# Performance work log

Hardware: AMD Instinct MI355X
Metric: run time of the kernel (lower is better)

The kernel has to match this reference:

```python
import jax, jax.numpy as jnp
import numpy as np

MIN_NORM = 1e-15
N = 10000        # num_nodes
E = 320000       # num edges (avg degree 32)
F_IN = 512       # in_features
HID = 256        # hardcoded encoder hidden dim
D_HYP = 2        # Poincare embedding dim
HEIGHT = 2
MAX_SIZE = 0.999
MIN_SCALE = HEIGHT * (MAX_SIZE / (HEIGHT + 1))  # = 0.666, scale clamp lower bound
MAX_SCALE = MAX_SIZE


def setup_inputs() -> dict:
    key = jax.random.key(0)
    ks = jax.random.split(key, 5)
    feature = jax.random.normal(ks[0], (N, F_IN), jnp.float32)
    edge_index = jax.random.randint(ks[1], (2, E), 0, N, dtype=jnp.int64)
    W1 = jax.random.normal(ks[2], (F_IN, HID), jnp.float32) / np.sqrt(F_IN).astype(np.float32)
    b1 = jnp.zeros((HID,), jnp.float32)
    W2 = jax.random.normal(ks[3], (HID, D_HYP), jnp.float32) / np.sqrt(HID).astype(np.float32)
    b2 = jnp.zeros((D_HYP,), jnp.float32)
    scale = jnp.ones((1,), jnp.float32)  # init_size overridden to 1.0 in __init__
    return {"feature": feature, "edge_index": edge_index, "W1": W1, "b1": b1,
            "W2": W2, "b2": b2, "scale": scale}


def _gcn_agg(h, src, dst):
    # symmetric-normalized edge_index gather/aggregate (message passing)
    deg = jax.ops.segment_sum(jnp.ones((src.shape[0],), h.dtype), dst, num_segments=N)
    deg = jnp.maximum(deg, 1.0)
    norm = jax.lax.rsqrt(deg[src] * deg[dst])            # [E]
    msg = h[src] * norm[:, None]                          # [E, C] gather (irregular)
    return jax.ops.segment_sum(msg, dst, num_segments=N)  # [N, C] scatter-add


def reference(feature, edge_index, W1, b1, W2, b2, scale):
    src, dst = edge_index[0], edge_index[1]
    # 2-layer graph encoder (linear -> aggregate -> relu, linear -> aggregate)
    h = jax.nn.relu(_gcn_agg(feature @ W1 + b1, src, dst))   # [N, HID]
    u = _gcn_agg(h @ W2 + b2, src, dst)                      # [N, D_HYP] tangent at origin
    # lift to Lorentz model (k=-1) via expmap0: x = [cosh|u|, sinh|u| * u/|u|]
    un = jnp.maximum(jnp.linalg.norm(u, axis=-1, keepdims=True), MIN_NORM)
    x_l = jnp.concatenate([jnp.cosh(un), jnp.sinh(un) * u / un], axis=-1)  # [N, D_HYP+1]
    # Lorentz -> Poincare: p = x_space / (1 + x_time)
    p = x_l[:, 1:] / (1.0 + x_l[:, :1])
    # normalize: F.normalize(p, dim=-1) * scale.clamp(min_size, max_size)
    pn = jnp.maximum(jnp.linalg.norm(p, axis=-1, keepdims=True), 1e-12)
    s = jnp.clip(scale, MIN_SCALE, MAX_SCALE)
    p = p / pn * s
    # project onto Poincare ball of curvature k=-1 with eps=MIN_NORM
    norm = jnp.maximum(jnp.linalg.norm(p, axis=-1, keepdims=True), MIN_NORM)
    maxnorm = 1.0 - MIN_NORM
    return jnp.where(norm > maxnorm, p / norm * maxnorm, p)
```

## Files before the change

kernel.cpp:

```cpp
#include <hip/hip_runtime.h>
#include <math.h>

#define N_NODES 10000
#define N_EDGES 320000
#define F_IN 512
#define HID 256
#define PAD_DEG 80
#define N_GEMM_BLKS 632
#define BUILD_BLKS ((N_EDGES + 255) / 256)

typedef _Float16 half8 __attribute__((ext_vector_type(8)));
typedef _Float16 half4v __attribute__((ext_vector_type(4)));
typedef float floatx4 __attribute__((ext_vector_type(4)));

typedef const __attribute__((address_space(1))) void* gas_ptr;
typedef __attribute__((address_space(3))) void* las_ptr;

__device__ __forceinline__ void dma16(const void* g, void* l) {
    __builtin_amdgcn_global_load_lds((gas_ptr)g, (las_ptr)l, 16, 0, 0);
}

__device__ __forceinline__ void fma4(float4& acc, float s, const float4& v) {
    acc.x += s * v.x; acc.y += s * v.y; acc.z += s * v.z; acc.w += s * v.w;
}

__device__ __forceinline__ float4 h4_to_f4(half4v h) {
    float4 f; f.x = (float)h[0]; f.y = (float)h[1]; f.z = (float)h[2]; f.w = (float)h[3];
    return f;
}


__global__ __launch_bounds__(256) void k_pre(const float* __restrict__ W1,
                                             int* __restrict__ count,
                                             _Float16* __restrict__ Bt_hi,
                                             _Float16* __restrict__ Bt_lo) {
    int i = blockIdx.x * blockDim.x + threadIdx.x;
    if (i < 10240) count[i] = 0;
    int k = i >> 8, n = i & 255;
    float v = W1[i];
    _Float16 hi = (_Float16)v;
    Bt_hi[n * F_IN + k] = hi;
    Bt_lo[n * F_IN + k] = (_Float16)(v - (float)hi);
}


__global__ __launch_bounds__(256) void k_main(const float* __restrict__ A,
                                              const _Float16* __restrict__ Bt_hi,
                                              const _Float16* __restrict__ Bt_lo,
                                              const float* __restrict__ b1,
                                              _Float16* __restrict__ h0h,
                                              const int* __restrict__ ei,
                                              int* __restrict__ count,
                                              int* __restrict__ csr) {
    __shared__ float    As[4][2048];
    __shared__ _Float16 Bhs[4][2048];
    __shared__ _Float16 Bls[4][2048];
    const int tid = threadIdx.x;

    if (blockIdx.x >= N_GEMM_BLKS) {
        int e = (blockIdx.x - N_GEMM_BLKS) * 256 + tid;
        if (e < N_EDGES) {
            int src = ei[e];
            int dst = ei[N_EDGES + e];
            int pos = atomicAdd(&count[dst], 1);
            csr[dst * PAD_DEG + pos] = src;
        }
        return;
    }

    const int b = blockIdx.x;
    const int t = (b & 7) * 79 + (b >> 3);
    const int row0 = (t >> 2) * 64, col0 = (t & 3) * 64;

    const int sA0 = tid, sA1 = tid + 256;
    const int rA0 = sA0 >> 3, hA0 = (sA0 & 7) ^ (rA0 & 7);
    const int rA1 = sA1 >> 3, hA1 = (sA1 & 7) ^ (rA1 & 7);
    int gr0 = row0 + rA0; if (gr0 > N_NODES - 1) gr0 = N_NODES - 1;
    int gr1 = row0 + rA1; if (gr1 > N_NODES - 1) gr1 = N_NODES - 1;
    const float* gA0 = A + (size_t)gr0 * F_IN + hA0 * 4;
    const float* gA1 = A + (size_t)gr1 * F_IN + hA1 * 4;
    const int cB = tid >> 2, hB = (tid & 3) ^ (cB & 3);
    const _Float16* gBh = Bt_hi + (size_t)(col0 + cB) * F_IN + hB * 8;
    const _Float16* gBl = Bt_lo + (size_t)(col0 + cB) * F_IN + hB * 8;

    const int wdma = __builtin_amdgcn_readfirstlane(tid >> 6);
    char* lA  = (char*)&As[0][0];
    char* lBh = (char*)&Bhs[0][0];
    char* lBl = (char*)&Bls[0][0];
    const int dA0u = wdma * 1024;
    const int dA1u = 4096 + wdma * 1024;
    const int dBu  = wdma * 1024;

    dma16(gA0, lA + dA0u);
    dma16(gA1, lA + dA1u);
    dma16(gBh, lBh + dBu);
    dma16(gBl, lBl + dBu);
    dma16(gA0 + 32, lA  + 8192 + dA0u);
    dma16(gA1 + 32, lA  + 8192 + dA1u);
    dma16(gBh + 32, lBh + 4096 + dBu);
    dma16(gBl + 32, lBl + 4096 + dBu);

    const int lane = tid & 63, w = tid >> 6;
    const int quad = lane >> 4, l15 = lane & 15;
    const int wm = (w >> 1) * 32, wn = (w & 1) * 32;
    floatx4 acc[2][2] = {};

    int aoff[2][2], boff[2];
    #pragma unroll
    for (int mi = 0; mi < 2; ++mi) {
        int r = wm + mi * 16 + l15;
        aoff[mi][0] = r * 128 + ((2 * quad)     ^ (r & 7)) * 16;
        aoff[mi][1] = r * 128 + ((2 * quad + 1) ^ (r & 7)) * 16;
    }
    #pragma unroll
    for (int ni = 0; ni < 2; ++ni) {
        int n = wn + ni * 16 + l15;
        boff[ni] = n * 64 + (quad ^ (n & 3)) * 16;
    }

    for (int it = 0; it < 16; ++it) {
        if (it < 15) asm volatile("s_waitcnt vmcnt(4)" ::: "memory");
        else         asm volatile("s_waitcnt vmcnt(0)" ::: "memory");
        __builtin_amdgcn_s_barrier();
        __builtin_amdgcn_sched_barrier(0);

        const int cb = it & 3;
        const char* bA = lA  + cb * 8192;
        const char* bH = lBh + cb * 4096;
        const char* bL = lBl + cb * 4096;
        half8 ah[2], al[2], bhf[2], blf[2];
        #pragma unroll
        for (int mi = 0; mi < 2; ++mi) {
            float4 f0 = *(const float4*)(bA + aoff[mi][0]);
            float4 f1 = *(const float4*)(bA + aoff[mi][1]);
            float av[8] = {f0.x, f0.y, f0.z, f0.w, f1.x, f1.y, f1.z, f1.w};
            #pragma unroll
            for (int j = 0; j < 8; ++j) {
                _Float16 h = (_Float16)av[j];
                ah[mi][j] = h;
                al[mi][j] = (_Float16)(av[j] - (float)h);
            }
        }
        #pragma unroll
        for (int ni = 0; ni < 2; ++ni) {
            bhf[ni] = *(const half8*)(bH + boff[ni]);
            blf[ni] = *(const half8*)(bL + boff[ni]);
        }
        #pragma unroll
        for (int ni = 0; ni < 2; ++ni)
            #pragma unroll
            for (int mi = 0; mi < 2; ++mi) {
                acc[mi][ni] = __builtin_amdgcn_mfma_f32_16x16x32_f16(ah[mi], bhf[ni], acc[mi][ni], 0, 0, 0);
                acc[mi][ni] = __builtin_amdgcn_mfma_f32_16x16x32_f16(ah[mi], blf[ni], acc[mi][ni], 0, 0, 0);
                acc[mi][ni] = __builtin_amdgcn_mfma_f32_16x16x32_f16(al[mi], bhf[ni], acc[mi][ni], 0, 0, 0);
            }

        if (it + 2 < 16) {
            const int k2 = (it + 2) * 32;
            const int nb = (it + 2) & 3;
            dma16(gA0 + k2, lA  + nb * 8192 + dA0u);
            dma16(gA1 + k2, lA  + nb * 8192 + dA1u);
            dma16(gBh + k2, lBh + nb * 4096 + dBu);
            dma16(gBl + k2, lBl + nb * 4096 + dBu);
        }
    }

    #pragma unroll
    for (int mi = 0; mi < 2; ++mi)
        #pragma unroll
        for (int ni = 0; ni < 2; ++ni) {
            int colb = col0 + wn + ni * 16 + l15;
            float bias = b1[colb];
            #pragma unroll
            for (int reg = 0; reg < 4; ++reg) {
                int rowb = row0 + wm + mi * 16 + quad * 4 + reg;
                if (rowb < N_NODES)
                    h0h[(size_t)rowb * HID + colb] = (_Float16)(acc[mi][ni][reg] + bias);
            }
        }
}


__global__ __launch_bounds__(256) void k_agg1(const _Float16* __restrict__ h0h,
                                              const int* __restrict__ csr,
                                              const int* __restrict__ count,
                                              const float* __restrict__ W2,
                                              const float* __restrict__ b2,
                                              float* __restrict__ u0) {
    __shared__ int2 nb[4][PAD_DEG];
    const int wid = threadIdx.x >> 6;
    const int lane = threadIdx.x & 63;
    const int n = blockIdx.x * 4 + wid;
    const int deg = count[n];
    const float degd = (float)(deg > 0 ? deg : 1);
    const int* row = csr + (size_t)n * PAD_DEG;
    for (int j = lane; j < deg; j += 64) {
        int s = row[j];
        int cs = count[s];
        float wq = rsqrtf((float)(cs > 0 ? cs : 1) * degd);
        nb[wid][j] = make_int2(s, __float_as_int(wq));
    }
    __syncthreads();

    const int off = lane << 2;
    float4 acc0 = {0,0,0,0}, acc1 = {0,0,0,0}, acc2 = {0,0,0,0}, acc3 = {0,0,0,0};
    int j = 0;
    for (; j + 16 <= deg; j += 16) {
        int2 e[16];
        #pragma unroll
        for (int q = 0; q < 16; ++q) e[q] = nb[wid][j + q];
        half4v v[16];
        #pragma unroll
        for (int q = 0; q < 16; ++q)
            v[q] = *(const half4v*)(h0h + ((size_t)e[q].x << 8) + off);
        #pragma unroll
        for (int q = 0; q < 16; q += 4) {
            fma4(acc0, __int_as_float(e[q + 0].y), h4_to_f4(v[q + 0]));
            fma4(acc1, __int_as_float(e[q + 1].y), h4_to_f4(v[q + 1]));
            fma4(acc2, __int_as_float(e[q + 2].y), h4_to_f4(v[q + 2]));
            fma4(acc3, __int_as_float(e[q + 3].y), h4_to_f4(v[q + 3]));
        }
    }
    for (; j + 4 <= deg; j += 4) {
        int2 e0 = nb[wid][j+0], e1 = nb[wid][j+1], e2 = nb[wid][j+2], e3 = nb[wid][j+3];
        half4v v0 = *(const half4v*)(h0h + ((size_t)e0.x << 8) + off);
        half4v v1 = *(const half4v*)(h0h + ((size_t)e1.x << 8) + off);
        half4v v2 = *(const half4v*)(h0h + ((size_t)e2.x << 8) + off);
        half4v v3 = *(const half4v*)(h0h + ((size_t)e3.x << 8) + off);
        fma4(acc0, __int_as_float(e0.y), h4_to_f4(v0));
        fma4(acc1, __int_as_float(e1.y), h4_to_f4(v1));
        fma4(acc2, __int_as_float(e2.y), h4_to_f4(v2));
        fma4(acc3, __int_as_float(e3.y), h4_to_f4(v3));
    }
    for (; j < deg; ++j) {
        int2 e = nb[wid][j];
        half4v v = *(const half4v*)(h0h + ((size_t)e.x << 8) + off);
        fma4(acc0, __int_as_float(e.y), h4_to_f4(v));
    }
    acc0.x += acc1.x + acc2.x + acc3.x;
    acc0.y += acc1.y + acc2.y + acc3.y;
    acc0.z += acc1.z + acc2.z + acc3.z;
    acc0.w += acc1.w + acc2.w + acc3.w;
    acc0.x = fmaxf(acc0.x, 0.f); acc0.y = fmaxf(acc0.y, 0.f);
    acc0.z = fmaxf(acc0.z, 0.f); acc0.w = fmaxf(acc0.w, 0.f);
    float4 wa = *(const float4*)(W2 + (lane << 3));
    float4 wb = *(const float4*)(W2 + (lane << 3) + 4);
    float p0 = acc0.x * wa.x + acc0.y * wa.z + acc0.z * wb.x + acc0.w * wb.z;
    float p1 = acc0.x * wa.y + acc0.y * wa.w + acc0.z * wb.y + acc0.w * wb.w;
    #pragma unroll
    for (int o = 32; o > 0; o >>= 1) {
        p0 += __shfl_down(p0, o);
        p1 += __shfl_down(p1, o);
    }
    if (lane == 0) {
        u0[2 * n]     = p0 + b2[0];
        u0[2 * n + 1] = p1 + b2[1];
    }
}


__global__ __launch_bounds__(256) void k_agg2(const float* __restrict__ u0,
                                              const int* __restrict__ csr,
                                              const int* __restrict__ count,
                                              const float* __restrict__ scale,
                                              float* __restrict__ out) {
    int n = blockIdx.x * 4 + (threadIdx.x >> 6);
    int lane = threadIdx.x & 63;
    if (n >= N_NODES) return;
    int deg = count[n];
    float degd = (float)(deg > 0 ? deg : 1);
    const int* row = csr + (size_t)n * PAD_DEG;
    float a0 = 0.f, a1 = 0.f;
    for (int j = lane; j < deg; j += 64) {
        int s = row[j];
        int cs = count[s];
        float wq = rsqrtf((float)(cs > 0 ? cs : 1) * degd);
        float2 uv = *(const float2*)(u0 + 2 * (size_t)s);
        a0 += wq * uv.x;
        a1 += wq * uv.y;
    }
    #pragma unroll
    for (int o = 32; o > 0; o >>= 1) {
        a0 += __shfl_down(a0, o);
        a1 += __shfl_down(a1, o);
    }
    if (lane == 0) {
        float un = fmaxf(sqrtf(a0 * a0 + a1 * a1), 1e-15f);
        float t = tanhf(0.5f * un) / un;
        float p0 = a0 * t, p1 = a1 * t;
        float pn = fmaxf(sqrtf(p0 * p0 + p1 * p1), 1e-12f);
        float s = fminf(fmaxf(scale[0], 0.666f), 0.999f);
        p0 = p0 / pn * s; p1 = p1 / pn * s;
        float nn = fmaxf(sqrtf(p0 * p0 + p1 * p1), 1e-15f);
        if (nn > 1.0f) { p0 = p0 / nn; p1 = p1 / nn; }
        out[2 * n]     = p0;
        out[2 * n + 1] = p1;
    }
}


extern "C" void kernel_launch(void* const* d_in, const int* in_sizes, int n_in,
                              void* d_out, int out_size, void* d_ws, size_t ws_size,
                              hipStream_t stream) {
    const float* feature = (const float*)d_in[0];
    const int*   ei      = (const int*)d_in[1];
    const float* W1      = (const float*)d_in[2];
    const float* b1      = (const float*)d_in[3];
    const float* W2      = (const float*)d_in[4];
    const float* b2      = (const float*)d_in[5];
    const float* scale   = (const float*)d_in[6];
    float* out = (float*)d_out;

    char* Wb = (char*)d_ws;
    int*      count = (int*)Wb;
    int*      csr   = (int*)(Wb + 40960);
    _Float16* h0h   = (_Float16*)(Wb + 3240960);
    float*    u0    = (float*)(Wb + 8360960);
    _Float16* Bt_hi = (_Float16*)(Wb + 8440960);
    _Float16* Bt_lo = (_Float16*)(Wb + 8703104);

    k_pre<<<dim3(512), dim3(256), 0, stream>>>(W1, count, Bt_hi, Bt_lo);
    k_main<<<dim3(N_GEMM_BLKS + BUILD_BLKS), dim3(256), 0, stream>>>(
        feature, Bt_hi, Bt_lo, b1, h0h, ei, count, csr);
    k_agg1<<<dim3((N_NODES + 3) / 4), dim3(256), 0, stream>>>(h0h, csr, count, W2, b2, u0);
    k_agg2<<<dim3((N_NODES + 3) / 4), dim3(256), 0, stream>>>(u0, csr, count, scale, out);
}
```

Before: 135.0 us.

## Build CSR via per-block histograms and prefix offsets instead of global atomics

```diff
diff --git a/kernel.cpp b/kernel.cpp
--- a/kernel.cpp
+++ b/kernel.cpp
@@ -7,7 +7,9 @@
 #define HID 256
 #define PAD_DEG 80
 #define N_GEMM_BLKS 632
-#define BUILD_BLKS ((N_EDGES + 255) / 256)
+#define CSR_BLKS 256
+#define EPB 1250
+#define NBIN 10240
 
 typedef _Float16 half8 __attribute__((ext_vector_type(8)));
 typedef _Float16 half4v __attribute__((ext_vector_type(4)));
@@ -44,29 +46,70 @@
 }
 
 
+__global__ __launch_bounds__(256) void k_csr1(const int* __restrict__ ei,
+                                              int* __restrict__ H) {
+    __shared__ int hist[NBIN];
+    const int tid = threadIdx.x, j = blockIdx.x;
+    for (int i = tid; i < NBIN; i += 256) hist[i] = 0;
+    __syncthreads();
+    const int e0 = j * EPB;
+    #pragma unroll
+    for (int q = 0; q < 5; ++q) {
+        int idx = q * 256 + tid;
+        if (idx < EPB) atomicAdd(&hist[ei[N_EDGES + e0 + idx]], 1);
+    }
+    __syncthreads();
+    for (int i = tid; i < NBIN; i += 256) H[j * NBIN + i] = hist[i];
+}
+
+
+__global__ __launch_bounds__(256) void k_csr2(int* __restrict__ H,
+                                              int* __restrict__ count) {
+    const int b = blockIdx.x * 256 + threadIdx.x;
+    int run = 0;
+    #pragma unroll 16
+    for (int j = 0; j < CSR_BLKS; ++j) {
+        int t = H[j * NBIN + b];
+        H[j * NBIN + b] = run;
+        run += t;
+    }
+    count[b] = run;
+}
+
+
 __global__ __launch_bounds__(256) void k_main(const float* __restrict__ A,
                                               const _Float16* __restrict__ Bt_hi,
                                               const _Float16* __restrict__ Bt_lo,
                                               const float* __restrict__ b1,
                                               _Float16* __restrict__ h0h,
                                               const int* __restrict__ ei,
-                                              int* __restrict__ count,
+                                              const int* __restrict__ H,
                                               int* __restrict__ csr) {
-    __shared__ float    As[4][2048];
-    __shared__ _Float16 Bhs[4][2048];
-    __shared__ _Float16 Bls[4][2048];
+    __shared__ __align__(16) char smem[65536];
     const int tid = threadIdx.x;
 
     if (blockIdx.x >= N_GEMM_BLKS) {
-        int e = (blockIdx.x - N_GEMM_BLKS) * 256 + tid;
-        if (e < N_EDGES) {
-            int src = ei[e];
-            int dst = ei[N_EDGES + e];
-            int pos = atomicAdd(&count[dst], 1);
-            csr[dst * PAD_DEG + pos] = src;
+        int* cur = (int*)smem;
+        const int j = blockIdx.x - N_GEMM_BLKS;
+        for (int i = tid; i < NBIN; i += 256) cur[i] = H[j * NBIN + i];
+        __syncthreads();
+        const int e0 = j * EPB;
+        #pragma unroll
+        for (int q = 0; q < 5; ++q) {
+            int idx = q * 256 + tid;
+            if (idx < EPB) {
+                int src = ei[e0 + idx];
+                int dst = ei[N_EDGES + e0 + idx];
+                int pos = atomicAdd(&cur[dst], 1);
+                csr[dst * PAD_DEG + pos] = src;
+            }
         }
         return;
     }
+
+    float    (*As)[2048]  = (float(*)[2048])smem;
+    _Float16 (*Bhs)[2048] = (_Float16(*)[2048])(smem + 32768);
+    _Float16 (*Bls)[2048] = (_Float16(*)[2048])(smem + 49152);
 
     const int b = blockIdx.x;
     const int t = (b & 7) * 79 + (b >> 3);
@@ -318,10 +361,13 @@
     float*    u0    = (float*)(Wb + 8360960);
     _Float16* Bt_hi = (_Float16*)(Wb + 8440960);
     _Float16* Bt_lo = (_Float16*)(Wb + 8703104);
+    int*      H     = (int*)(Wb + 8965248);
 
     k_pre<<<dim3(512), dim3(256), 0, stream>>>(W1, count, Bt_hi, Bt_lo);
-    k_main<<<dim3(N_GEMM_BLKS + BUILD_BLKS), dim3(256), 0, stream>>>(
-        feature, Bt_hi, Bt_lo, b1, h0h, ei, count, csr);
+    k_csr1<<<dim3(CSR_BLKS), dim3(256), 0, stream>>>(ei, H);
+    k_csr2<<<dim3(NBIN / 256), dim3(256), 0, stream>>>(H, count);
+    k_main<<<dim3(N_GEMM_BLKS + CSR_BLKS), dim3(256), 0, stream>>>(
+        feature, Bt_hi, Bt_lo, b1, h0h, ei, H, csr);
     k_agg1<<<dim3((N_NODES + 3) / 4), dim3(256), 0, stream>>>(h0h, csr, count, W2, b2, u0);
     k_agg2<<<dim3((N_NODES + 3) / 4), dim3(256), 0, stream>>>(u0, csr, count, scale, out);
 }
```

Measured after the change: 141.6 us. +4.9%, slower.

## Pre-split feature matrix into fp16 hi/lo in prep kernel before GEMM

Applied to the files above, without the earlier changes.

```diff
diff --git a/kernel.cpp b/kernel.cpp
--- a/kernel.cpp
+++ b/kernel.cpp
@@ -8,6 +8,8 @@
 #define PAD_DEG 80
 #define N_GEMM_BLKS 632
 #define BUILD_BLKS ((N_EDGES + 255) / 256)
+#define PRE_W1_BLKS 512
+#define PRE_A_BLKS 2500
 
 typedef _Float16 half8 __attribute__((ext_vector_type(8)));
 typedef _Float16 half4v __attribute__((ext_vector_type(4)));
@@ -31,20 +33,41 @@
 
 
 __global__ __launch_bounds__(256) void k_pre(const float* __restrict__ W1,
+                                             const float* __restrict__ A,
                                              int* __restrict__ count,
                                              _Float16* __restrict__ Bt_hi,
-                                             _Float16* __restrict__ Bt_lo) {
-    int i = blockIdx.x * blockDim.x + threadIdx.x;
-    if (i < 10240) count[i] = 0;
-    int k = i >> 8, n = i & 255;
-    float v = W1[i];
-    _Float16 hi = (_Float16)v;
-    Bt_hi[n * F_IN + k] = hi;
-    Bt_lo[n * F_IN + k] = (_Float16)(v - (float)hi);
-}
-
-
-__global__ __launch_bounds__(256) void k_main(const float* __restrict__ A,
+                                             _Float16* __restrict__ Bt_lo,
+                                             _Float16* __restrict__ Ahi,
+                                             _Float16* __restrict__ Alo) {
+    const int b = blockIdx.x, tid = threadIdx.x;
+    if (b < PRE_W1_BLKS) {
+        int i = b * 256 + tid;
+        if (i < 10240) count[i] = 0;
+        int k = i >> 8, n = i & 255;
+        float v = W1[i];
+        _Float16 hi = (_Float16)v;
+        Bt_hi[n * F_IN + k] = hi;
+        Bt_lo[n * F_IN + k] = (_Float16)(v - (float)hi);
+    } else {
+        int i = ((b - PRE_W1_BLKS) * 256 + tid) * 8;
+        float4 v0 = *(const float4*)(A + i);
+        float4 v1 = *(const float4*)(A + i + 4);
+        float av[8] = {v0.x, v0.y, v0.z, v0.w, v1.x, v1.y, v1.z, v1.w};
+        half8 h, l;
+        #pragma unroll
+        for (int j = 0; j < 8; ++j) {
+            _Float16 hh = (_Float16)av[j];
+            h[j] = hh;
+            l[j] = (_Float16)(av[j] - (float)hh);
+        }
+        *(half8*)(Ahi + i) = h;
+        *(half8*)(Alo + i) = l;
+    }
+}
+
+
+__global__ __launch_bounds__(256) void k_main(const _Float16* __restrict__ Ahi,
+                                              const _Float16* __restrict__ Alo,
                                               const _Float16* __restrict__ Bt_hi,
                                               const _Float16* __restrict__ Bt_lo,
                                               const float* __restrict__ b1,
@@ -52,7 +75,8 @@
                                               const int* __restrict__ ei,
                                               int* __restrict__ count,
                                               int* __restrict__ csr) {
-    __shared__ float    As[4][2048];
+    __shared__ _Float16 Ahs[4][2048];
+    __shared__ _Float16 Als[4][2048];
     __shared__ _Float16 Bhs[4][2048];
     __shared__ _Float16 Bls[4][2048];
     const int tid = threadIdx.x;
@@ -72,45 +96,39 @@
     const int t = (b & 7) * 79 + (b >> 3);
     const int row0 = (t >> 2) * 64, col0 = (t & 3) * 64;
 
-    const int sA0 = tid, sA1 = tid + 256;
-    const int rA0 = sA0 >> 3, hA0 = (sA0 & 7) ^ (rA0 & 7);
-    const int rA1 = sA1 >> 3, hA1 = (sA1 & 7) ^ (rA1 & 7);
-    int gr0 = row0 + rA0; if (gr0 > N_NODES - 1) gr0 = N_NODES - 1;
-    int gr1 = row0 + rA1; if (gr1 > N_NODES - 1) gr1 = N_NODES - 1;
-    const float* gA0 = A + (size_t)gr0 * F_IN + hA0 * 4;
-    const float* gA1 = A + (size_t)gr1 * F_IN + hA1 * 4;
-    const int cB = tid >> 2, hB = (tid & 3) ^ (cB & 3);
-    const _Float16* gBh = Bt_hi + (size_t)(col0 + cB) * F_IN + hB * 8;
-    const _Float16* gBl = Bt_lo + (size_t)(col0 + cB) * F_IN + hB * 8;
+    const int rS = tid >> 2, hS = (tid & 3) ^ (rS & 3);
+    int grA = row0 + rS; if (grA > N_NODES - 1) grA = N_NODES - 1;
+    const _Float16* gAh = Ahi + (size_t)grA * F_IN + hS * 8;
+    const _Float16* gAl = Alo + (size_t)grA * F_IN + hS * 8;
+    const _Float16* gBh = Bt_hi + (size_t)(col0 + rS) * F_IN + hS * 8;
+    const _Float16* gBl = Bt_lo + (size_t)(col0 + rS) * F_IN + hS * 8;
 
     const int wdma = __builtin_amdgcn_readfirstlane(tid >> 6);
-    char* lA  = (char*)&As[0][0];
+    char* lAh = (char*)&Ahs[0][0];
+    char* lAl = (char*)&Als[0][0];
     char* lBh = (char*)&Bhs[0][0];
     char* lBl = (char*)&Bls[0][0];
-    const int dA0u = wdma * 1024;
-    const int dA1u = 4096 + wdma * 1024;
-    const int dBu  = wdma * 1024;
-
-    dma16(gA0, lA + dA0u);
-    dma16(gA1, lA + dA1u);
-    dma16(gBh, lBh + dBu);
-    dma16(gBl, lBl + dBu);
-    dma16(gA0 + 32, lA  + 8192 + dA0u);
-    dma16(gA1 + 32, lA  + 8192 + dA1u);
-    dma16(gBh + 32, lBh + 4096 + dBu);
-    dma16(gBl + 32, lBl + 4096 + dBu);
+    const int dU = wdma * 1024;
+
+    dma16(gAh, lAh + dU);
+    dma16(gAl, lAl + dU);
+    dma16(gBh, lBh + dU);
+    dma16(gBl, lBl + dU);
+    dma16(gAh + 32, lAh + 4096 + dU);
+    dma16(gAl + 32, lAl + 4096 + dU);
+    dma16(gBh + 32, lBh + 4096 + dU);
+    dma16(gBl + 32, lBl + 4096 + dU);
 
     const int lane = tid & 63, w = tid >> 6;
     const int quad = lane >> 4, l15 = lane & 15;
     const int wm = (w >> 1) * 32, wn = (w & 1) * 32;
     floatx4 acc[2][2] = {};
 
-    int aoff[2][2], boff[2];
+    int aoff[2], boff[2];
     #pragma unroll
     for (int mi = 0; mi < 2; ++mi) {
         int r = wm + mi * 16 + l15;
-        aoff[mi][0] = r * 128 + ((2 * quad)     ^ (r & 7)) * 16;
-        aoff[mi][1] = r * 128 + ((2 * quad + 1) ^ (r & 7)) * 16;
+        aoff[mi] = r * 64 + (quad ^ (r & 3)) * 16;
     }
     #pragma unroll
     for (int ni = 0; ni < 2; ++ni) {
@@ -125,26 +143,16 @@
         __builtin_amdgcn_sched_barrier(0);
 
         const int cb = it & 3;
-        const char* bA = lA  + cb * 8192;
-        const char* bH = lBh + cb * 4096;
-        const char* bL = lBl + cb * 4096;
         half8 ah[2], al[2], bhf[2], blf[2];
         #pragma unroll
         for (int mi = 0; mi < 2; ++mi) {
-            float4 f0 = *(const float4*)(bA + aoff[mi][0]);
-            float4 f1 = *(const float4*)(bA + aoff[mi][1]);
-            float av[8] = {f0.x, f0.y, f0.z, f0.w, f1.x, f1.y, f1.z, f1.w};
-            #pragma unroll
-            for (int j = 0; j < 8; ++j) {
-                _Float16 h = (_Float16)av[j];
-                ah[mi][j] = h;
-                al[mi][j] = (_Float16)(av[j] - (float)h);
-            }
+            ah[mi] = *(const half8*)(lAh + cb * 4096 + aoff[mi]);
+            al[mi] = *(const half8*)(lAl + cb * 4096 + aoff[mi]);
         }
         #pragma unroll
         for (int ni = 0; ni < 2; ++ni) {
-            bhf[ni] = *(const half8*)(bH + boff[ni]);
-            blf[ni] = *(const half8*)(bL + boff[ni]);
+            bhf[ni] = *(const half8*)(lBh + cb * 4096 + boff[ni]);
+            blf[ni] = *(const half8*)(lBl + cb * 4096 + boff[ni]);
         }
         #pragma unroll
         for (int ni = 0; ni < 2; ++ni)
@@ -158,10 +166,10 @@
         if (it + 2 < 16) {
             const int k2 = (it + 2) * 32;
             const int nb = (it + 2) & 3;
-            dma16(gA0 + k2, lA  + nb * 8192 + dA0u);
-            dma16(gA1 + k2, lA  + nb * 8192 + dA1u);
-            dma16(gBh + k2, lBh + nb * 4096 + dBu);
-            dma16(gBl + k2, lBl + nb * 4096 + dBu);
+            dma16(gAh + k2, lAh + nb * 4096 + dU);
+            dma16(gAl + k2, lAl + nb * 4096 + dU);
+            dma16(gBh + k2, lBh + nb * 4096 + dU);
+            dma16(gBl + k2, lBl + nb * 4096 + dU);
         }
     }
 
@@ -318,10 +326,13 @@
     float*    u0    = (float*)(Wb + 8360960);
     _Float16* Bt_hi = (_Float16*)(Wb + 8440960);
     _Float16* Bt_lo = (_Float16*)(Wb + 8703104);
-
-    k_pre<<<dim3(512), dim3(256), 0, stream>>>(W1, count, Bt_hi, Bt_lo);
+    _Float16* Ahi   = (_Float16*)(Wb + 8965248);
+    _Float16* Alo   = (_Float16*)(Wb + 19205248);
+
+    k_pre<<<dim3(PRE_W1_BLKS + PRE_A_BLKS), dim3(256), 0, stream>>>(
+        W1, feature, count, Bt_hi, Bt_lo, Ahi, Alo);
     k_main<<<dim3(N_GEMM_BLKS + BUILD_BLKS), dim3(256), 0, stream>>>(
-        feature, Bt_hi, Bt_lo, b1, h0h, ei, count, csr);
+        Ahi, Alo, Bt_hi, Bt_lo, b1, h0h, ei, count, csr);
     k_agg1<<<dim3((N_NODES + 3) / 4), dim3(256), 0, stream>>>(h0h, csr, count, W2, b2, u0);
     k_agg2<<<dim3((N_NODES + 3) / 4), dim3(256), 0, stream>>>(u0, csr, count, scale, out);
 }
```

Result: slower. 139.7 us (+3.4%).
